# Performance work log

Measured on AMD Instinct MI355X. Metric: run time of the kernel, lower is better.

Reference implementation:

```python
import jax, jax.numpy as jnp
import numpy as np

B, L, E, S = 4, 1024, 256, 32  # batch, seq_len, e_dim, local window half-size
NEG = -1e30  # stands in for excluding out-of-range positions from softmax


def setup_inputs() -> dict:
    key = jax.random.key(0)
    ks = jax.random.split(key, 8)
    sc = 1.0 / np.sqrt(E)
    return {
        "q": jax.random.normal(ks[0], (B, L, E), jnp.float32),
        "Wq": jax.random.normal(ks[1], (E, E), jnp.float32) * sc,
        "bq": jax.random.normal(ks[2], (E,), jnp.float32) * sc,
        "Wk": jax.random.normal(ks[3], (E, E), jnp.float32) * sc,
        "bk": jax.random.normal(ks[4], (E,), jnp.float32) * sc,
        "Wv": jax.random.normal(ks[5], (E, E), jnp.float32) * sc,
        "bv": jax.random.normal(ks[6], (E,), jnp.float32) * sc,
        "pos_bias": jax.random.normal(ks[7], (2 * S + 1, E), jnp.float32),
    }


def reference(q, Wq, bq, Wk, bk, Wv, bv, pos_bias):
    # Linear projections (nn.Linear: x @ W.T + b)
    Q = q @ Wq.T + bq
    K = q @ Wk.T + bk
    V = q @ Wv.T + bv

    W = 2 * S + 1
    rel = jnp.arange(-S, S + 1)                      # [W] relative offsets
    idx = jnp.arange(L)[:, None] + rel[None, :]       # [L, W] absolute positions
    valid = (idx >= 0) & (idx < L)                    # in-sequence window entries
    idxc = jnp.clip(idx, 0, L - 1)
    strict = jnp.abs(rel) < S                         # |j-i| < s mask (zeroes K at edges)

    # Gather windows: [B, L, W, E]
    K_win = K[:, idxc] + pos_bias[rel + S][None, None, :, :]
    K_masked = jnp.where(strict[None, None, :, None], K_win, 0.0)
    # Out-of-range positions excluded from softmax entirely (logit -> -inf)
    logits = jnp.where(valid[None, :, :, None], Q[:, :, None, :] * K_masked, NEG)
    weights = jax.nn.softmax(logits, axis=2)          # per-channel softmax over window

    V_win = jnp.where(valid[None, :, :, None], V[:, idxc], 0.0)
    ctx = jnp.sum(weights * V_win, axis=2)            # [B, L, E]

    sig = jax.nn.sigmoid(Q)
    # sigmoid applied inside the loop and again at the end -> squared
    return sig * sig * ctx
```

## Files before the change

### kernel.cpp

```cpp
#include <hip/hip_runtime.h>
#include <hip/hip_bf16.h>

#define B_ 4
#define L_ 1024
#define E_ 256
#define S_ 32

typedef __bf16 bf16x8 __attribute__((ext_vector_type(8)));
typedef float f32x4 __attribute__((ext_vector_type(4)));

__device__ __forceinline__ __bf16 bf_from_bits(unsigned short u) {
    __bf16 b;
    __builtin_memcpy(&b, &u, 2);
    return b;
}

__device__ __forceinline__ void load8split(const float* __restrict__ p,
                                           bf16x8& h, bf16x8& l) {
    const float4 x0 = *(const float4*)p;
    const float4 x1 = *(const float4*)(p + 4);
    const float xs[8] = {x0.x, x0.y, x0.z, x0.w, x1.x, x1.y, x1.z, x1.w};
#pragma unroll
    for (int j = 0; j < 8; ++j) {
        const unsigned hb = __float_as_uint(xs[j]) & 0xFFFF0000u;
        h[j] = bf_from_bits((unsigned short)(hb >> 16));
        l[j] = (__bf16)(xs[j] - __uint_as_float(hb));
    }
}

__global__ __launch_bounds__(256, 1) void qkv_gemm2(
    const float* __restrict__ A,
    const float* __restrict__ Wq, const float* __restrict__ bq,
    const float* __restrict__ Wk, const float* __restrict__ bk,
    const float* __restrict__ Wv, const float* __restrict__ bv,
    float* __restrict__ Qo, float* __restrict__ Ko, float* __restrict__ Vo)
{
    const float* Wm;
    const float* bm;
    float* Om;
    const int z = blockIdx.z;
    if (z == 0)      { Wm = Wq; bm = bq; Om = Qo; }
    else if (z == 1) { Wm = Wk; bm = bk; Om = Ko; }
    else             { Wm = Wv; bm = bv; Om = Vo; }

    const int wave = threadIdx.x >> 6;
    const int lane = threadIdx.x & 63;
    const int rsel = lane & 15;
    const int koff = (lane >> 4) * 8;

    const int m0 = blockIdx.x * 32;
    const int nb = wave * 64;

    const float* pa0 = A + (size_t)(m0 + rsel) * 256 + koff;
    const float* pa1 = pa0 + (size_t)16 * 256;
    const float* pw0 = Wm + (size_t)(nb + 0  + rsel) * 256 + koff;
    const float* pw1 = Wm + (size_t)(nb + 16 + rsel) * 256 + koff;
    const float* pw2 = Wm + (size_t)(nb + 32 + rsel) * 256 + koff;
    const float* pw3 = Wm + (size_t)(nb + 48 + rsel) * 256 + koff;

    f32x4 acc[2][4];
#pragma unroll
    for (int mt = 0; mt < 2; ++mt)
#pragma unroll
        for (int nt = 0; nt < 4; ++nt)
            acc[mt][nt] = (f32x4){0.f, 0.f, 0.f, 0.f};

#pragma unroll
    for (int k0 = 0; k0 < 256; k0 += 32) {
        bf16x8 ah[2], al[2], bh[4], bl[4];
        load8split(pa0 + k0, ah[0], al[0]);
        load8split(pa1 + k0, ah[1], al[1]);
        load8split(pw0 + k0, bh[0], bl[0]);
        load8split(pw1 + k0, bh[1], bl[1]);
        load8split(pw2 + k0, bh[2], bl[2]);
        load8split(pw3 + k0, bh[3], bl[3]);
#pragma unroll
        for (int mt = 0; mt < 2; ++mt)
#pragma unroll
            for (int nt = 0; nt < 4; ++nt) {
                acc[mt][nt] = __builtin_amdgcn_mfma_f32_16x16x32_bf16(
                    ah[mt], bh[nt], acc[mt][nt], 0, 0, 0);
                acc[mt][nt] = __builtin_amdgcn_mfma_f32_16x16x32_bf16(
                    ah[mt], bl[nt], acc[mt][nt], 0, 0, 0);
                acc[mt][nt] = __builtin_amdgcn_mfma_f32_16x16x32_bf16(
                    al[mt], bh[nt], acc[mt][nt], 0, 0, 0);
            }
    }

#pragma unroll
    for (int mt = 0; mt < 2; ++mt) {
        const int mrow = m0 + mt * 16 + (lane >> 4) * 4;
#pragma unroll
        for (int nt = 0; nt < 4; ++nt) {
            const int n = nb + nt * 16 + rsel;
            const float bias = bm[n];
#pragma unroll
            for (int r = 0; r < 4; ++r)
                Om[(size_t)(mrow + r) * 256 + n] = acc[mt][nt][r] + bias;
        }
    }
}

#define TI2 32
#define CH2 64
#define HB2 96
#define PS2 68

__global__ __launch_bounds__(256) void aft_stage2b(
    const float* __restrict__ Q, const float* __restrict__ K,
    const float* __restrict__ V, const float* __restrict__ pb,
    float* __restrict__ out)
{
    __shared__ float Kw[HB2][PS2];
    __shared__ float Vw[HB2][PS2];
    __shared__ float Pw[2 * S_ + 1][PS2];

    const int tid = threadIdx.x;
    const int b  = blockIdx.y;
    const int i0 = blockIdx.x * TI2;
    const int c0 = blockIdx.z * CH2;

    const float* Kb = K + (size_t)b * L_ * E_;
    const float* Vb = V + (size_t)b * L_ * E_;

    for (int idx = tid; idx < HB2 * 16; idx += 256) {
        const int r  = idx >> 4;
        const int cq = (idx & 15) * 4;
        int j = i0 - S_ + r;
        j = j < 0 ? 0 : (j > L_ - 1 ? L_ - 1 : j);
        const size_t g = (size_t)j * E_ + c0 + cq;
        *(float4*)&Kw[r][cq] = *(const float4*)(Kb + g);
        *(float4*)&Vw[r][cq] = *(const float4*)(Vb + g);
    }
    for (int idx = tid; idx < (2 * S_ + 1) * 16; idx += 256) {
        const int r  = idx >> 4;
        const int cq = (idx & 15) * 4;
        *(float4*)&Pw[r][cq] = *(const float4*)(pb + (size_t)r * E_ + c0 + cq);
    }
    __syncthreads();

    const int cq = (tid & 15) * 4;
    const int is = tid >> 4;

#pragma unroll
    for (int rep = 0; rep < 2; ++rep) {
        const int rr = is + rep * 16;
        const int i  = i0 + rr;

        const float4 qv = *(const float4*)(Q + ((size_t)b * L_ + i) * E_ + c0 + cq);

        float den0 = 0.f, den1 = 0.f, den2 = 0.f, den3 = 0.f;
        float num0 = 0.f, num1 = 0.f, num2 = 0.f, num3 = 0.f;

        const int jlo = (i - S_ < 0) ? 0 : (i - S_);
        const int jhi = (i + S_ > L_ - 1) ? (L_ - 1) : (i + S_);

        for (int j = jlo; j <= jhi; ++j) {
            const int r = j - (i0 - S_);
            const int w = j - i + S_;
            const float4 vv = *(const float4*)&Vw[r][cq];

            float kx = 0.f, ky = 0.f, kz = 0.f, kw = 0.f;
            if (w != 0 && w != 2 * S_) {
                const float4 kk = *(const float4*)&Kw[r][cq];
                const float4 pp = *(const float4*)&Pw[w][cq];
                kx = kk.x + pp.x;
                ky = kk.y + pp.y;
                kz = kk.z + pp.z;
                kw = kk.w + pp.w;
            }
            const float e0 = __expf(qv.x * kx);
            const float e1 = __expf(qv.y * ky);
            const float e2 = __expf(qv.z * kz);
            const float e3 = __expf(qv.w * kw);
            den0 += e0; den1 += e1; den2 += e2; den3 += e3;
            num0 += e0 * vv.x; num1 += e1 * vv.y;
            num2 += e2 * vv.z; num3 += e3 * vv.w;
        }

        const float s0 = 1.f / (1.f + __expf(-qv.x));
        const float s1 = 1.f / (1.f + __expf(-qv.y));
        const float s2 = 1.f / (1.f + __expf(-qv.z));
        const float s3 = 1.f / (1.f + __expf(-qv.w));

        float4 o;
        o.x = s0 * s0 * num0 / den0;
        o.y = s1 * s1 * num1 / den1;
        o.z = s2 * s2 * num2 / den2;
        o.w = s3 * s3 * num3 / den3;
        *(float4*)(out + ((size_t)b * L_ + i) * E_ + c0 + cq) = o;
    }
}

#define TI 32
#define CG 64
#define RK 96
#define LDP 68

__global__ __launch_bounds__(256) void aft_fused(
    const float* __restrict__ q,
    const float* __restrict__ Wq, const float* __restrict__ bq,
    const float* __restrict__ Wk, const float* __restrict__ bk,
    const float* __restrict__ Wv, const float* __restrict__ bv,
    const float* __restrict__ pb,
    float* __restrict__ out)
{
    __shared__ float Kl[RK][LDP];
    __shared__ float Vl[RK][LDP];
    __shared__ float Ql[TI][LDP];

    const int i0 = blockIdx.x * TI;
    const int b  = blockIdx.y;
    const int c0 = blockIdx.z * CG;

    const int wave = threadIdx.x >> 6;
    const int lane = threadIdx.x & 63;
    const int rsel = lane & 15;
    const int koff = (lane >> 4) * 8;

    const float* qb = q + (size_t)b * L_ * E_;

    for (int job = wave; job < 56; job += 4) {
        int p, rt, ct;
        if (job < 24)      { p = 0; rt = job >> 2;        ct = job & 3; }
        else if (job < 48) { p = 1; rt = (job - 24) >> 2; ct = (job - 24) & 3; }
        else               { p = 2; rt = (job - 48) >> 2; ct = (job - 48) & 3; }

        int jrow = (p == 2) ? (i0 + rt * 16 + rsel)
                            : (i0 - S_ + rt * 16 + rsel);
        int jc = jrow < 0 ? 0 : (jrow > L_ - 1 ? L_ - 1 : jrow);
        const float* pa = qb + (size_t)jc * E_ + koff;

        const float* Wm = (p == 0) ? Wk : (p == 1) ? Wv : Wq;
        const float* bm = (p == 0) ? bk : (p == 1) ? bv : bq;
        const int n = c0 + ct * 16 + rsel;
        const float* pw = Wm + (size_t)n * E_ + koff;

        f32x4 acc = {0.f, 0.f, 0.f, 0.f};
#pragma unroll
        for (int k0 = 0; k0 < 256; k0 += 32) {
            bf16x8 ah, al, bh, bl;
            load8split(pa + k0, ah, al);
            load8split(pw + k0, bh, bl);
            acc = __builtin_amdgcn_mfma_f32_16x16x32_bf16(ah, bh, acc, 0, 0, 0);
            acc = __builtin_amdgcn_mfma_f32_16x16x32_bf16(ah, bl, acc, 0, 0, 0);
            acc = __builtin_amdgcn_mfma_f32_16x16x32_bf16(al, bh, acc, 0, 0, 0);
        }

        const float bias = bm[n];
        const int row0 = rt * 16 + (lane >> 4) * 4;
        const int colc = ct * 16 + rsel;
        float* dst = (p == 0) ? &Kl[0][0] : (p == 1) ? &Vl[0][0] : &Ql[0][0];
#pragma unroll
        for (int r = 0; r < 4; ++r)
            dst[(size_t)(row0 + r) * LDP + colc] = acc[r] + bias;
    }
    __syncthreads();

    const int cq  = threadIdx.x & 15;
    const int is0 = threadIdx.x >> 4;
    const int cL  = cq * 4;
    const int cG  = c0 + cL;
    const float* pbc = pb + cG;

    for (int rr = is0; rr < TI; rr += 16) {
        const int i = i0 + rr;
        const float4 qv = *(const float4*)&Ql[rr][cL];

        float den0 = 0.f, den1 = 0.f, den2 = 0.f, den3 = 0.f;
        float num0 = 0.f, num1 = 0.f, num2 = 0.f, num3 = 0.f;

        const int jlo = (i - S_ < 0) ? 0 : (i - S_);
        const int jhi = (i + S_ > L_ - 1) ? (L_ - 1) : (i + S_);

        for (int j = jlo; j <= jhi; ++j) {
            const int r = j - (i0 - S_);
            const int w = j - i + S_;
            const float4 vv = *(const float4*)&Vl[r][cL];

            float kx = 0.f, ky = 0.f, kz = 0.f, kw = 0.f;
            if (w != 0 && w != 2 * S_) {
                const float4 kk = *(const float4*)&Kl[r][cL];
                const float4 pp = *(const float4*)(pbc + (size_t)w * E_);
                kx = kk.x + pp.x;
                ky = kk.y + pp.y;
                kz = kk.z + pp.z;
                kw = kk.w + pp.w;
            }
            const float e0 = __expf(qv.x * kx);
            const float e1 = __expf(qv.y * ky);
            const float e2 = __expf(qv.z * kz);
            const float e3 = __expf(qv.w * kw);
            den0 += e0; den1 += e1; den2 += e2; den3 += e3;
            num0 += e0 * vv.x; num1 += e1 * vv.y;
            num2 += e2 * vv.z; num3 += e3 * vv.w;
        }

        const float s0 = 1.f / (1.f + __expf(-qv.x));
        const float s1 = 1.f / (1.f + __expf(-qv.y));
        const float s2 = 1.f / (1.f + __expf(-qv.z));
        const float s3 = 1.f / (1.f + __expf(-qv.w));

        float4 o;
        o.x = s0 * s0 * num0 / den0;
        o.y = s1 * s1 * num1 / den1;
        o.z = s2 * s2 * num2 / den2;
        o.w = s3 * s3 * num3 / den3;
        *(float4*)(out + ((size_t)b * L_ + i) * E_ + cG) = o;
    }
}

extern "C" void kernel_launch(void* const* d_in, const int* in_sizes, int n_in,
                              void* d_out, int out_size, void* d_ws, size_t ws_size,
                              hipStream_t stream) {
    const float* q  = (const float*)d_in[0];
    const float* Wq = (const float*)d_in[1];
    const float* bq = (const float*)d_in[2];
    const float* Wk = (const float*)d_in[3];
    const float* bk = (const float*)d_in[4];
    const float* Wv = (const float*)d_in[5];
    const float* bv = (const float*)d_in[6];
    const float* pb = (const float*)d_in[7];

    const size_t needA = (size_t)3 * 4096 * 256 * sizeof(float);

    if (ws_size >= needA) {
        float* Qf = (float*)d_ws;
        float* Kf = Qf + (size_t)4096 * 256;
        float* Vf = Kf + (size_t)4096 * 256;
        qkv_gemm2<<<dim3(128, 1, 3), 256, 0, stream>>>(q, Wq, bq, Wk, bk, Wv, bv,
                                                       Qf, Kf, Vf);
        aft_stage2b<<<dim3(L_ / TI2, B_, E_ / CH2), 256, 0, stream>>>(
            Qf, Kf, Vf, pb, (float*)d_out);
    } else {
        aft_fused<<<dim3(L_ / TI, B_, E_ / CG), 256, 0, stream>>>(
            q, Wq, bq, Wk, bk, Wv, bv, pb, (float*)d_out);
    }
}
```

Baseline: 123.6 us.

## Presplit GEMM inputs to bf16 hi/lo and pair rows in window attention

Adds a presplit kernel that converts the input and weights into bf16 high/low halves once, so the QKV GEMM reads bf16 directly instead of splitting fp32 on every tile load. The GEMM launch bounds are relaxed to allow two blocks per CU. The attention stage now has each thread handle two adjacent rows that share K/V loads, uses exp2 with a pre-scaled Q, and takes an interior fast path that drops per-element edge and validity checks. The cost is an extra kernel launch and extra workspace traffic for the split arrays.

```diff
diff --git a/kernel.cpp b/kernel.cpp
--- a/kernel.cpp
+++ b/kernel.cpp
@@ -13,6 +13,16 @@
     __bf16 b;
     __builtin_memcpy(&b, &u, 2);
     return b;
+}
+
+__device__ __forceinline__ void split1(float x, unsigned short& h, unsigned short& l) {
+    const unsigned u  = __float_as_uint(x);
+    const unsigned hb = u & 0xFFFF0000u;
+    h = (unsigned short)(hb >> 16);
+    __bf16 lo = (__bf16)(x - __uint_as_float(hb));
+    unsigned short lu;
+    __builtin_memcpy(&lu, &lo, 2);
+    l = lu;
 }
 
 __device__ __forceinline__ void load8split(const float* __restrict__ p,
@@ -23,25 +33,55 @@
 #pragma unroll
     for (int j = 0; j < 8; ++j) {
         const unsigned hb = __float_as_uint(xs[j]) & 0xFFFF0000u;
-        h[j] = bf_from_bits((unsigned short)(hb >> 16));
+        h[j] = bf_from_bits((unsigned short)(__float_as_uint(xs[j]) >> 16));
         l[j] = (__bf16)(xs[j] - __uint_as_float(hb));
     }
 }
 
-__global__ __launch_bounds__(256, 1) void qkv_gemm2(
+__global__ __launch_bounds__(256) void presplit(
     const float* __restrict__ A,
-    const float* __restrict__ Wq, const float* __restrict__ bq,
-    const float* __restrict__ Wk, const float* __restrict__ bk,
-    const float* __restrict__ Wv, const float* __restrict__ bv,
+    const float* __restrict__ Wq, const float* __restrict__ Wk,
+    const float* __restrict__ Wv,
+    unsigned short* __restrict__ Ah, unsigned short* __restrict__ Al,
+    unsigned short* __restrict__ Wh, unsigned short* __restrict__ Wl)
+{
+    const int e8 = (blockIdx.x * 256 + threadIdx.x) * 8;
+    const float* src;
+    unsigned short* dh;
+    unsigned short* dl;
+    if (e8 < 1048576) {
+        src = A + e8; dh = Ah + e8; dl = Al + e8;
+    } else {
+        const int r = e8 - 1048576;
+        const int m = r >> 16;
+        const int o = r & 65535;
+        src = (m == 0 ? Wq : m == 1 ? Wk : Wv) + o;
+        dh = Wh + r; dl = Wl + r;
+    }
+    const float4 x0 = *(const float4*)src;
+    const float4 x1 = *(const float4*)(src + 4);
+    const float xs[8] = {x0.x, x0.y, x0.z, x0.w, x1.x, x1.y, x1.z, x1.w};
+    unsigned short hs[8], ls[8];
+#pragma unroll
+    for (int j = 0; j < 8; ++j) split1(xs[j], hs[j], ls[j]);
+    *(ushort4*)(dh)     = make_ushort4(hs[0], hs[1], hs[2], hs[3]);
+    *(ushort4*)(dh + 4) = make_ushort4(hs[4], hs[5], hs[6], hs[7]);
+    *(ushort4*)(dl)     = make_ushort4(ls[0], ls[1], ls[2], ls[3]);
+    *(ushort4*)(dl + 4) = make_ushort4(ls[4], ls[5], ls[6], ls[7]);
+}
+
+__global__ __launch_bounds__(256, 2) void qkv_gemm3(
+    const unsigned short* __restrict__ Ah, const unsigned short* __restrict__ Al,
+    const unsigned short* __restrict__ Wh, const unsigned short* __restrict__ Wl,
+    const float* __restrict__ bq, const float* __restrict__ bk,
+    const float* __restrict__ bv,
     float* __restrict__ Qo, float* __restrict__ Ko, float* __restrict__ Vo)
 {
-    const float* Wm;
-    const float* bm;
-    float* Om;
     const int z = blockIdx.z;
-    if (z == 0)      { Wm = Wq; bm = bq; Om = Qo; }
-    else if (z == 1) { Wm = Wk; bm = bk; Om = Ko; }
-    else             { Wm = Wv; bm = bv; Om = Vo; }
+    const float* bm = (z == 0) ? bq : (z == 1) ? bk : bv;
+    float* Om       = (z == 0) ? Qo : (z == 1) ? Ko : Vo;
+    const unsigned short* Whz = Wh + (size_t)z * 65536;
+    const unsigned short* Wlz = Wl + (size_t)z * 65536;
 
     const int wave = threadIdx.x >> 6;
     const int lane = threadIdx.x & 63;
@@ -51,12 +91,19 @@
     const int m0 = blockIdx.x * 32;
     const int nb = wave * 64;
 
-    const float* pa0 = A + (size_t)(m0 + rsel) * 256 + koff;
-    const float* pa1 = pa0 + (size_t)16 * 256;
-    const float* pw0 = Wm + (size_t)(nb + 0  + rsel) * 256 + koff;
-    const float* pw1 = Wm + (size_t)(nb + 16 + rsel) * 256 + koff;
-    const float* pw2 = Wm + (size_t)(nb + 32 + rsel) * 256 + koff;
-    const float* pw3 = Wm + (size_t)(nb + 48 + rsel) * 256 + koff;
+    const unsigned short* pa0h = Ah + (size_t)(m0 + rsel) * 256 + koff;
+    const unsigned short* pa0l = Al + (size_t)(m0 + rsel) * 256 + koff;
+    const unsigned short* pa1h = pa0h + 16 * 256;
+    const unsigned short* pa1l = pa0l + 16 * 256;
+
+    const unsigned short* pwh[4];
+    const unsigned short* pwl[4];
+#pragma unroll
+    for (int nt = 0; nt < 4; ++nt) {
+        const size_t off = (size_t)(nb + nt * 16 + rsel) * 256 + koff;
+        pwh[nt] = Whz + off;
+        pwl[nt] = Wlz + off;
+    }
 
     f32x4 acc[2][4];
 #pragma unroll
@@ -68,12 +115,15 @@
 #pragma unroll
     for (int k0 = 0; k0 < 256; k0 += 32) {
         bf16x8 ah[2], al[2], bh[4], bl[4];
-        load8split(pa0 + k0, ah[0], al[0]);
-        load8split(pa1 + k0, ah[1], al[1]);
-        load8split(pw0 + k0, bh[0], bl[0]);
-        load8split(pw1 + k0, bh[1], bl[1]);
-        load8split(pw2 + k0, bh[2], bl[2]);
-        load8split(pw3 + k0, bh[3], bl[3]);
+        ah[0] = *(const bf16x8*)(pa0h + k0);
+        al[0] = *(const bf16x8*)(pa0l + k0);
+        ah[1] = *(const bf16x8*)(pa1h + k0);
+        al[1] = *(const bf16x8*)(pa1l + k0);
+#pragma unroll
+        for (int nt = 0; nt < 4; ++nt) {
+            bh[nt] = *(const bf16x8*)(pwh[nt] + k0);
+            bl[nt] = *(const bf16x8*)(pwl[nt] + k0);
+        }
 #pragma unroll
         for (int mt = 0; mt < 2; ++mt)
 #pragma unroll
@@ -105,8 +155,9 @@
 #define CH2 64
 #define HB2 96
 #define PS2 68
-
-__global__ __launch_bounds__(256) void aft_stage2b(
+#define LOG2E 1.4426950408889634f
+
+__global__ __launch_bounds__(256) void aft_stage2c(
     const float* __restrict__ Q, const float* __restrict__ K,
     const float* __restrict__ V, const float* __restrict__ pb,
     float* __restrict__ out)
@@ -140,55 +191,130 @@
     __syncthreads();
 
     const int cq = (tid & 15) * 4;
-    const int is = tid >> 4;
-
-#pragma unroll
-    for (int rep = 0; rep < 2; ++rep) {
-        const int rr = is + rep * 16;
-        const int i  = i0 + rr;
-
-        const float4 qv = *(const float4*)(Q + ((size_t)b * L_ + i) * E_ + c0 + cq);
-
-        float den0 = 0.f, den1 = 0.f, den2 = 0.f, den3 = 0.f;
-        float num0 = 0.f, num1 = 0.f, num2 = 0.f, num3 = 0.f;
-
-        const int jlo = (i - S_ < 0) ? 0 : (i - S_);
-        const int jhi = (i + S_ > L_ - 1) ? (L_ - 1) : (i + S_);
-
-        for (int j = jlo; j <= jhi; ++j) {
-            const int r = j - (i0 - S_);
-            const int w = j - i + S_;
-            const float4 vv = *(const float4*)&Vw[r][cq];
-
-            float kx = 0.f, ky = 0.f, kz = 0.f, kw = 0.f;
-            if (w != 0 && w != 2 * S_) {
-                const float4 kk = *(const float4*)&Kw[r][cq];
-                const float4 pp = *(const float4*)&Pw[w][cq];
-                kx = kk.x + pp.x;
-                ky = kk.y + pp.y;
-                kz = kk.z + pp.z;
-                kw = kk.w + pp.w;
+    const int t  = tid >> 4;
+    const int i1 = i0 + 2 * t;
+    const int i2 = i1 + 1;
+    const int r0 = 2 * t;
+
+    const float4 qa = *(const float4*)(Q + ((size_t)b * L_ + i1) * E_ + c0 + cq);
+    const float4 qb2 = *(const float4*)(Q + ((size_t)b * L_ + i2) * E_ + c0 + cq);
+    const float4 q2a = make_float4(qa.x * LOG2E, qa.y * LOG2E, qa.z * LOG2E, qa.w * LOG2E);
+    const float4 q2b = make_float4(qb2.x * LOG2E, qb2.y * LOG2E, qb2.z * LOG2E, qb2.w * LOG2E);
+
+    float4 den1 = {0, 0, 0, 0}, num1 = {0, 0, 0, 0};
+    float4 den2 = {0, 0, 0, 0}, num2 = {0, 0, 0, 0};
+
+    const bool interior = (blockIdx.x >= 1) && (blockIdx.x <= (L_ / TI2) - 2);
+
+    if (interior) {
+        {
+            const float4 v = *(const float4*)&Vw[r0][cq];
+            den1.x += 1.f; den1.y += 1.f; den1.z += 1.f; den1.w += 1.f;
+            num1.x += v.x; num1.y += v.y; num1.z += v.z; num1.w += v.w;
+        }
+        float4 p_old;
+        {
+            const float4 p = *(const float4*)&Pw[1][cq];
+            const float4 k = *(const float4*)&Kw[r0 + 1][cq];
+            const float4 v = *(const float4*)&Vw[r0 + 1][cq];
+            const float e0 = __builtin_amdgcn_exp2f(q2a.x * (k.x + p.x));
+            const float e1 = __builtin_amdgcn_exp2f(q2a.y * (k.y + p.y));
+            const float e2 = __builtin_amdgcn_exp2f(q2a.z * (k.z + p.z));
+            const float e3 = __builtin_amdgcn_exp2f(q2a.w * (k.w + p.w));
+            den1.x += e0; den1.y += e1; den1.z += e2; den1.w += e3;
+            num1.x += e0 * v.x; num1.y += e1 * v.y; num1.z += e2 * v.z; num1.w += e3 * v.w;
+            den2.x += 1.f; den2.y += 1.f; den2.z += 1.f; den2.w += 1.f;
+            num2.x += v.x; num2.y += v.y; num2.z += v.z; num2.w += v.w;
+            p_old = p;
+        }
+        for (int w1 = 2; w1 <= 63; ++w1) {
+            const float4 p = *(const float4*)&Pw[w1][cq];
+            const float4 k = *(const float4*)&Kw[r0 + w1][cq];
+            const float4 v = *(const float4*)&Vw[r0 + w1][cq];
+            const float a0 = __builtin_amdgcn_exp2f(q2a.x * (k.x + p.x));
+            const float a1 = __builtin_amdgcn_exp2f(q2a.y * (k.y + p.y));
+            const float a2 = __builtin_amdgcn_exp2f(q2a.z * (k.z + p.z));
+            const float a3 = __builtin_amdgcn_exp2f(q2a.w * (k.w + p.w));
+            const float b0 = __builtin_amdgcn_exp2f(q2b.x * (k.x + p_old.x));
+            const float b1 = __builtin_amdgcn_exp2f(q2b.y * (k.y + p_old.y));
+            const float b2 = __builtin_amdgcn_exp2f(q2b.z * (k.z + p_old.z));
+            const float b3 = __builtin_amdgcn_exp2f(q2b.w * (k.w + p_old.w));
+            den1.x += a0; den1.y += a1; den1.z += a2; den1.w += a3;
+            num1.x += a0 * v.x; num1.y += a1 * v.y; num1.z += a2 * v.z; num1.w += a3 * v.w;
+            den2.x += b0; den2.y += b1; den2.z += b2; den2.w += b3;
+            num2.x += b0 * v.x; num2.y += b1 * v.y; num2.z += b2 * v.z; num2.w += b3 * v.w;
+            p_old = p;
+        }
+        {
+            const float4 k = *(const float4*)&Kw[r0 + 64][cq];
+            const float4 v = *(const float4*)&Vw[r0 + 64][cq];
+            den1.x += 1.f; den1.y += 1.f; den1.z += 1.f; den1.w += 1.f;
+            num1.x += v.x; num1.y += v.y; num1.z += v.z; num1.w += v.w;
+            const float b0 = __builtin_amdgcn_exp2f(q2b.x * (k.x + p_old.x));
+            const float b1 = __builtin_amdgcn_exp2f(q2b.y * (k.y + p_old.y));
+            const float b2 = __builtin_amdgcn_exp2f(q2b.z * (k.z + p_old.z));
+            const float b3 = __builtin_amdgcn_exp2f(q2b.w * (k.w + p_old.w));
+            den2.x += b0; den2.y += b1; den2.z += b2; den2.w += b3;
+            num2.x += b0 * v.x; num2.y += b1 * v.y; num2.z += b2 * v.z; num2.w += b3 * v.w;
+        }
+        {
+            const float4 v = *(const float4*)&Vw[r0 + 65][cq];
+            den2.x += 1.f; den2.y += 1.f; den2.z += 1.f; den2.w += 1.f;
+            num2.x += v.x; num2.y += v.y; num2.z += v.z; num2.w += v.w;
+        }
+    } else {
+#pragma unroll
+        for (int rowsel = 0; rowsel < 2; ++rowsel) {
+            const int i = rowsel ? i2 : i1;
+            const float4 q2 = rowsel ? q2b : q2a;
+            float4* den = rowsel ? &den2 : &den1;
+            float4* num = rowsel ? &num2 : &num1;
+            for (int w = 0; w <= 64; ++w) {
+                const int j = i - S_ + w;
+                const bool valid = (unsigned)j < (unsigned)L_;
+                const int r = (i - i0) + w;
+                const float4 k = *(const float4*)&Kw[r][cq];
+                const float4 v = *(const float4*)&Vw[r][cq];
+                const float4 p = *(const float4*)&Pw[w][cq];
+                const bool edge = (w == 0) || (w == 64);
+                const float lx = edge ? 0.f : q2.x * (k.x + p.x);
+                const float ly = edge ? 0.f : q2.y * (k.y + p.y);
+                const float lz = edge ? 0.f : q2.z * (k.z + p.z);
+                const float lw = edge ? 0.f : q2.w * (k.w + p.w);
+                const float e0 = valid ? __builtin_amdgcn_exp2f(lx) : 0.f;
+                const float e1 = valid ? __builtin_amdgcn_exp2f(ly) : 0.f;
+                const float e2 = valid ? __builtin_amdgcn_exp2f(lz) : 0.f;
+                const float e3 = valid ? __builtin_amdgcn_exp2f(lw) : 0.f;
+                den->x += e0; den->y += e1; den->z += e2; den->w += e3;
+                num->x += e0 * v.x; num->y += e1 * v.y;
+                num->z += e2 * v.z; num->w += e3 * v.w;
             }
-            const float e0 = __expf(qv.x * kx);
-            const float e1 = __expf(qv.y * ky);
-            const float e2 = __expf(qv.z * kz);
-            const float e3 = __expf(qv.w * kw);
-            den0 += e0; den1 += e1; den2 += e2; den3 += e3;
-            num0 += e0 * vv.x; num1 += e1 * vv.y;
-            num2 += e2 * vv.z; num3 += e3 * vv.w;
-        }
-
-        const float s0 = 1.f / (1.f + __expf(-qv.x));
-        const float s1 = 1.f / (1.f + __expf(-qv.y));
-        const float s2 = 1.f / (1.f + __expf(-qv.z));
-        const float s3 = 1.f / (1.f + __expf(-qv.w));
-
+        }
+    }
+
+    {
+        const float s0 = 1.f / (1.f + __builtin_amdgcn_exp2f(-q2a.x));
+        const float s1 = 1.f / (1.f + __builtin_amdgcn_exp2f(-q2a.y));
+        const float s2 = 1.f / (1.f + __builtin_amdgcn_exp2f(-q2a.z));
+        const float s3 = 1.f / (1.f + __builtin_amdgcn_exp2f(-q2a.w));
         float4 o;
-        o.x = s0 * s0 * num0 / den0;
-        o.y = s1 * s1 * num1 / den1;
-        o.z = s2 * s2 * num2 / den2;
-        o.w = s3 * s3 * num3 / den3;
-        *(float4*)(out + ((size_t)b * L_ + i) * E_ + c0 + cq) = o;
+        o.x = s0 * s0 * num1.x / den1.x;
+        o.y = s1 * s1 * num1.y / den1.y;
+        o.z = s2 * s2 * num1.z / den1.z;
+        o.w = s3 * s3 * num1.w / den1.w;
+        *(float4*)(out + ((size_t)b * L_ + i1) * E_ + c0 + cq) = o;
+    }
+    {
+        const float s0 = 1.f / (1.f + __builtin_amdgcn_exp2f(-q2b.x));
+        const float s1 = 1.f / (1.f + __builtin_amdgcn_exp2f(-q2b.y));
+        const float s2 = 1.f / (1.f + __builtin_amdgcn_exp2f(-q2b.z));
+        const float s3 = 1.f / (1.f + __builtin_amdgcn_exp2f(-q2b.w));
+        float4 o;
+        o.x = s0 * s0 * num2.x / den2.x;
+        o.y = s1 * s1 * num2.y / den2.y;
+        o.z = s2 * s2 * num2.z / den2.z;
+        o.w = s3 * s3 * num2.w / den2.w;
+        *(float4*)(out + ((size_t)b * L_ + i2) * E_ + c0 + cq) = o;
     }
 }
 
@@ -322,15 +448,22 @@
     const float* bv = (const float*)d_in[6];
     const float* pb = (const float*)d_in[7];
 
-    const size_t needA = (size_t)3 * 4096 * 256 * sizeof(float);
+    const size_t needA = (size_t)3 * 1048576 * 4 + (size_t)2 * 1048576 * 2
+                       + (size_t)2 * 196608 * 2;
 
     if (ws_size >= needA) {
         float* Qf = (float*)d_ws;
-        float* Kf = Qf + (size_t)4096 * 256;
-        float* Vf = Kf + (size_t)4096 * 256;
-        qkv_gemm2<<<dim3(128, 1, 3), 256, 0, stream>>>(q, Wq, bq, Wk, bk, Wv, bv,
-                                                       Qf, Kf, Vf);
-        aft_stage2b<<<dim3(L_ / TI2, B_, E_ / CH2), 256, 0, stream>>>(
+        float* Kf = Qf + 1048576;
+        float* Vf = Kf + 1048576;
+        unsigned short* Ah = (unsigned short*)(Vf + 1048576);
+        unsigned short* Al = Ah + 1048576;
+        unsigned short* Wh = Al + 1048576;
+        unsigned short* Wl = Wh + 196608;
+
+        presplit<<<dim3(608), 256, 0, stream>>>(q, Wq, Wk, Wv, Ah, Al, Wh, Wl);
+        qkv_gemm3<<<dim3(128, 1, 3), 256, 0, stream>>>(Ah, Al, Wh, Wl,
+                                                       bq, bk, bv, Qf, Kf, Vf);
+        aft_stage2c<<<dim3(L_ / TI2, B_, E_ / CH2), 256, 0, stream>>>(
             Qf, Kf, Vf, pb, (float*)d_out);
     } else {
         aft_fused<<<dim3(L_ / TI, B_, E_ / CG), 256, 0, stream>>>(
```

Result: slower. 126.7 us (+2.5%).
